# Kernel tuning notes

Hardware: AMD Instinct MI355X
Metric: run time of the kernel (lower is better)

## Reference

```python
import jax, jax.numpy as jnp
import numpy as np

N = 10000        # num_nodes
F_IN = 256       # dataset_num_features
H = 128          # hidden_channels
C_OUT = 40       # dataset_num_classes
L = 3            # num_layers
HEADS = 8
DH = H // HEADS  # per-head dim
E = 160000       # num edges (before self loops)
SCALE = 1.0 / float(np.sqrt(DH))


def setup_inputs() -> dict:
    key = jax.random.key(0)
    ks = jax.random.split(key, 8)
    s = lambda k, *sh: (jax.random.normal(k, sh, dtype=jnp.float32) * 0.05)
    return dict(
        edge_index=jax.random.randint(ks[0], (2, E), 0, N, dtype=jnp.int32),
        x_param=s(ks[1], N, F_IN),
        lin1_w=s(ks[2], F_IN, H),
        lin1_b=jnp.zeros((H,), jnp.float32),
        wq=s(ks[3], L, H, H),
        wk=s(ks[4], L, H, H),
        wv=s(ks[5], L, H, H),
        bq=jnp.zeros((L, H), jnp.float32),
        bk=jnp.zeros((L, H), jnp.float32),
        bv=jnp.zeros((L, H), jnp.float32),
        lin2_w=s(ks[6], H, C_OUT),
        lin2_b=jnp.zeros((C_OUT,), jnp.float32),
    )


def _gcn_norm(edge_index):
    # PyG gcn_norm: add self loops (weight 1), symmetric D^-1/2 A D^-1/2
    loops = jnp.arange(N, dtype=edge_index.dtype)
    row = jnp.concatenate([edge_index[0], loops])  # source j
    col = jnp.concatenate([edge_index[1], loops])  # target i
    deg = jax.ops.segment_sum(jnp.ones(row.shape, jnp.float32), col, num_segments=N)
    dis = jnp.where(deg > 0, jax.lax.rsqrt(jnp.maximum(deg, 1e-12)), 0.0)
    return row, col, dis[row] * dis[col]


def _restricted_softmax(score):
    # softmax with an implicit extra logit at `margin=0`
    m = jnp.maximum(jnp.max(score, axis=-1, keepdims=True), 0.0)
    e = jnp.exp(score - m)
    return e / (jnp.sum(e, axis=-1, keepdims=True) + jnp.exp(-m))


def _forward(edge_index, x_param, lin1_w, lin1_b, wq, wk, wv, bq, bk, bv, lin2_w, lin2_b):
    row, col, norm = _gcn_norm(edge_index)
    # dropouts are eval-mode no-ops
    x = jax.nn.relu(x_param @ lin1_w + lin1_b)  # [N, H]
    x_all = x[:, None, :]                       # [N, 1, H]
    for l in range(L):
        t = x_all.shape[1]
        # project per-node first (linear commutes with per-edge gather)
        q = (x_all[:, -1] @ wq[l] + bq[l]).reshape(N, HEADS, DH)      # query from latest state
        k = (x_all @ wk[l] + bk[l]).reshape(N, t, HEADS, DH)          # keys over full history
        v = (x_all @ wv[l] + bv[l]).reshape(N, t, HEADS, DH)
        qe = q[col]   # [Etot, heads, dh]   (x_i)
        ke = k[row]   # [Etot, t, heads, dh] (x_j)
        ve = v[row]
        score = jnp.einsum('ehd,ethd->eht', qe, ke) * SCALE
        attn = _restricted_softmax(score)        # attention-dropout is a no-op in eval
        msg = jnp.einsum('eht,ethd->ehd', attn, ve).reshape(-1, H) * norm[:, None]
        out = jax.ops.segment_sum(msg, col, num_segments=N)  # aggr='add'
        x = jax.nn.relu(out)
        x_all = jnp.concatenate([x_all, x[:, None, :]], axis=1)
    logits = x_all[:, -1] @ lin2_w + lin2_b
    return jax.nn.log_softmax(logits, axis=1)


def reference(edge_index, x_param, lin1_w, lin1_b, wq, wk, wv, bq, bk, bv, lin2_w, lin2_b):
    return _forward(edge_index, x_param, lin1_w, lin1_b, wq, wk, wv, bq, bk, bv, lin2_w, lin2_b)
```

## Files before the change

### kernel.cpp

```cpp
#include <hip/hip_runtime.h>
#include <math.h>

#define N_NODES 10000
#define F_IN_D  256
#define H_DIM   128
#define C_OUTD  40
#define NHEADS  8
#define NEDGES  160000
#define ETOT    (NEDGES + N_NODES)
#define SCALE_F 0.25f
#define TILES_N 157

typedef __attribute__((ext_vector_type(8))) short bf16x8;
typedef __attribute__((ext_vector_type(4))) float f32x4;
typedef __attribute__((ext_vector_type(2))) float f32x2;

__device__ __forceinline__ unsigned short f2bf(float f) {
    unsigned int u = __float_as_uint(f);
    unsigned int r = (u + 0x7FFFu + ((u >> 16) & 1u)) >> 16;
    return (unsigned short)r;
}
__device__ __forceinline__ float bf2f(unsigned short h) {
    return __uint_as_float(((unsigned int)h) << 16);
}
__device__ __forceinline__ unsigned char f2fp8(float v) {
    int pk = __builtin_amdgcn_cvt_pk_fp8_f32(v, v, 0, false);
    return (unsigned char)(pk & 0xff);
}


__global__ void k_scan(int* __restrict__ degi, int* __restrict__ offsets) {
    __shared__ int part[1024];
    int tid = threadIdx.x;
    int s = 0;
    if (tid < 1000) {
        int beg = tid * 10;
        #pragma unroll
        for (int i = 0; i < 10; ++i) s += degi[beg + i] + 1;
    }
    part[tid] = s;
    __syncthreads();
    for (int off = 1; off < 1024; off <<= 1) {
        int v = 0;
        if (tid >= off) v = part[tid - off];
        __syncthreads();
        part[tid] += v;
        __syncthreads();
    }
    if (tid < 1000) {
        int base = part[tid] - s;
        int beg = tid * 10;
        #pragma unroll
        for (int i = 0; i < 10; ++i) {
            int d = degi[beg + i] + 1;
            offsets[beg + i] = base;
            degi[beg + i]    = d;
            base += d;
        }
    }
}

__global__ void k_scatter(const int* __restrict__ row, const int* __restrict__ col,
                          const int* __restrict__ degi, const int* __restrict__ offsets,
                          int* cursor, int* csr_row, float* csr_norm) {
    int e = blockIdx.x * 256 + threadIdx.x;
    if (e >= ETOT) return;
    int r, c;
    if (e < NEDGES) { r = row[e]; c = col[e]; }
    else            { r = c = e - NEDGES; }
    int slot = offsets[c] + atomicAdd(&cursor[c], 1);
    float dr = rsqrtf((float)degi[r]);
    float dc = rsqrtf((float)degi[c]);
    csr_row[slot]  = r;
    csr_norm[slot] = dr * dc;
}


__global__ void k_prep(const float* __restrict__ w1, const float* __restrict__ wq,
                       const float* __restrict__ wk, const float* __restrict__ wv,
                       const float* __restrict__ w2, const int* __restrict__ col,
                       unsigned short* __restrict__ W1T, unsigned short* __restrict__ WTq,
                       unsigned short* __restrict__ WTk, unsigned short* __restrict__ WTv,
                       unsigned short* __restrict__ W2T, int* __restrict__ degi) {
    int b = blockIdx.x;
    if (b < 728) {
        int e = b * 256 + threadIdx.x;
        if (e < 32768) {
            int n = e >> 8, k = e & 255;
            W1T[e] = f2bf(w1[k * H_DIM + n]);
        } else if (e < 180224) {
            int e2 = e - 32768;
            int mat = e2 >> 14;
            int r   = e2 & 16383;
            int n = r >> 7, k = r & 127;
            int l = mat / 3, ws = mat % 3;
            const float*    src = (ws == 0) ? wq  : (ws == 1) ? wk  : wv;
            unsigned short* dst = (ws == 0) ? WTq : (ws == 1) ? WTk : WTv;
            dst[l * 16384 + n * H_DIM + k] = f2bf(src[l * 16384 + k * H_DIM + n]);
        } else if (e < 186368) {
            int e3 = e - 180224;
            int c = e3 >> 7, k = e3 & 127;
            W2T[c * H_DIM + k] = (c < C_OUTD) ? f2bf(w2[k * C_OUTD + c]) : 0;
        }
    } else {
        int e = (b - 728) * 256 + threadIdx.x;
        if (e < NEDGES) atomicAdd(&degi[col[e]], 1);
    }
}


__global__ __launch_bounds__(256) void k_lin1_mfma(const float* __restrict__ X,
                                                   const unsigned short* __restrict__ W1T,
                                                   const float* __restrict__ b1,
                                                   unsigned short* __restrict__ X0,
                                                   int nct) {
    int tid = threadIdx.x;
    int wid = tid >> 6, lane = tid & 63;
    int m = lane & 15, quad = lane >> 4;
    int rowA = blockIdx.x * 64 + wid * 16 + m;
    int rowc = rowA < N_NODES ? rowA : N_NODES - 1;
    bf16x8 af[8];
    const float* ap = X + (size_t)rowc * F_IN_D + quad * 8;
    #pragma unroll
    for (int s = 0; s < 8; ++s) {
        float4 lo = *(const float4*)(ap + s * 32);
        float4 hi = *(const float4*)(ap + s * 32 + 4);
        union { unsigned short u[8]; bf16x8 v; } pk;
        pk.u[0] = f2bf(lo.x); pk.u[1] = f2bf(lo.y);
        pk.u[2] = f2bf(lo.z); pk.u[3] = f2bf(lo.w);
        pk.u[4] = f2bf(hi.x); pk.u[5] = f2bf(hi.y);
        pk.u[6] = f2bf(hi.z); pk.u[7] = f2bf(hi.w);
        af[s] = pk.v;
    }
    int row0 = blockIdx.x * 64 + wid * 16 + quad * 4;
    for (int ct = 0; ct < nct; ++ct) {
        int col = ct * 16 + m;
        const unsigned short* bp = W1T + (size_t)col * F_IN_D + quad * 8;
        f32x4 acc = {0.f, 0.f, 0.f, 0.f};
        #pragma unroll
        for (int s = 0; s < 8; ++s) {
            bf16x8 bfr = __builtin_bit_cast(bf16x8, *(const uint4*)(bp + s * 32));
            acc = __builtin_amdgcn_mfma_f32_16x16x32_bf16(af[s], bfr, acc, 0, 0, 0);
        }
        float bb = b1[col];
        #pragma unroll
        for (int rg = 0; rg < 4; ++rg) {
            int r = row0 + rg;
            if (r < N_NODES)
                X0[(size_t)r * H_DIM + col] = f2bf(fmaxf(acc[rg] + bb, 0.f));
        }
    }
}


__global__ __launch_bounds__(256) void k_qkv_mfma(const unsigned short* __restrict__ XHb,
                                                  const unsigned short* __restrict__ WTq,
                                                  const unsigned short* __restrict__ WTk,
                                                  const unsigned short* __restrict__ WTv,
                                                  const float* __restrict__ bq,
                                                  const float* __restrict__ bk,
                                                  const float* __restrict__ bv,
                                                  unsigned short* __restrict__ Qb,
                                                  unsigned char* __restrict__ KVb,
                                                  int l, int t, int nct) {
    int tid = threadIdx.x;
    int wid = tid >> 6, lane = tid & 63;
    int m = lane & 15, quad = lane >> 4;
    int mi = blockIdx.x / TILES_N;
    int rt = blockIdx.x % TILES_N;
    const unsigned short* WT; const float* bias; int slice, mode;
    if (mi == 0)      { WT = WTq; bias = bq; slice = l;          mode = 0; }
    else if (mi <= t) { WT = WTk; bias = bk; slice = mi - 1;     mode = 1; }
    else              { WT = WTv; bias = bv; slice = mi - t - 1; mode = 2; }
    const unsigned short* A = XHb + (size_t)slice * N_NODES * H_DIM;
    int rowA = rt * 64 + wid * 16 + m;
    bf16x8 af[4];
    const unsigned short* ap = A + (size_t)rowA * H_DIM + quad * 8;
    #pragma unroll
    for (int s = 0; s < 4; ++s)
        af[s] = __builtin_bit_cast(bf16x8, *(const uint4*)(ap + s * 32));
    int row0 = rt * 64 + wid * 16 + quad * 4;
    int vofs = (mode == 2) ? 8 : 0;
    for (int cp = 0; cp < nct; ++cp) {
        int colA = cp * 32 + m;
        int colB = colA + 16;
        const unsigned short* bpA = WT + (size_t)colA * H_DIM + quad * 8;
        const unsigned short* bpB = WT + (size_t)colB * H_DIM + quad * 8;
        bf16x8 bA[4], bB[4];
        #pragma unroll
        for (int s = 0; s < 4; ++s) {
            bA[s] = __builtin_bit_cast(bf16x8, *(const uint4*)(bpA + s * 32));
            bB[s] = __builtin_bit_cast(bf16x8, *(const uint4*)(bpB + s * 32));
        }
        f32x4 accA = {0.f, 0.f, 0.f, 0.f};
        f32x4 accB = {0.f, 0.f, 0.f, 0.f};
        #pragma unroll
        for (int s = 0; s < 4; ++s) {
            accA = __builtin_amdgcn_mfma_f32_16x16x32_bf16(af[s], bA[s], accA, 0, 0, 0);
            accB = __builtin_amdgcn_mfma_f32_16x16x32_bf16(af[s], bB[s], accB, 0, 0, 0);
        }
        float bbA = bias[colA], bbB = bias[colB];
        #pragma unroll
        for (int rg = 0; rg < 4; ++rg) {
            int r = row0 + rg;
            if (r < N_NODES) {
                float vA = accA[rg] + bbA;
                float vB = accB[rg] + bbB;
                if (mode == 0) {
                    Qb[(size_t)r * H_DIM + colA] = f2bf(vA);
                    Qb[(size_t)r * H_DIM + colB] = f2bf(vB);
                } else {
                    size_t nb = ((size_t)r * 3 + slice) * 256;
                    KVb[nb + (colA >> 3) * 16 + (colA & 7) + vofs] = f2fp8(vA);
                    KVb[nb + (colB >> 3) * 16 + (colB & 7) + vofs] = f2fp8(vB);
                }
            }
        }
    }
}


template <int T>
__device__ __forceinline__ void kv_load(const uint4* __restrict__ KV, int r, int ci,
                                        uint4 (&kv)[T]) {
    const uint4* p = KV + (size_t)r * 48 + ci;
    #pragma unroll
    for (int s = 0; s < T; ++s) kv[s] = p[s * 16];
}

template <int T>
__device__ __forceinline__ void edge_accum(const uint4 (&kv)[T], const float (&q)[8],
                                           float nrm, float (&a)[8]) {
    float sc[T];
    #pragma unroll
    for (int s = 0; s < T; ++s) {
        f32x2 k0 = __builtin_amdgcn_cvt_pk_f32_fp8(kv[s].x, false);
        f32x2 k1 = __builtin_amdgcn_cvt_pk_f32_fp8(kv[s].x, true);
        f32x2 k2 = __builtin_amdgcn_cvt_pk_f32_fp8(kv[s].y, false);
        f32x2 k3 = __builtin_amdgcn_cvt_pk_f32_fp8(kv[s].y, true);
        float p = q[0] * k0[0] + q[1] * k0[1] + q[2] * k1[0] + q[3] * k1[1]
                + q[4] * k2[0] + q[5] * k2[1] + q[6] * k3[0] + q[7] * k3[1];
        p += __shfl_xor(p, 1, 2);
        sc[s] = p;
    }
    float m = 0.f;
    #pragma unroll
    for (int s = 0; s < T; ++s) m = fmaxf(m, sc[s]);
    float den = __expf(-m);
    float mv[8];
    #pragma unroll
    for (int i = 0; i < 8; ++i) mv[i] = 0.f;
    #pragma unroll
    for (int s = 0; s < T; ++s) {
        float w = __expf(sc[s] - m);
        den += w;
        f32x2 v0 = __builtin_amdgcn_cvt_pk_f32_fp8(kv[s].z, false);
        f32x2 v1 = __builtin_amdgcn_cvt_pk_f32_fp8(kv[s].z, true);
        f32x2 v2 = __builtin_amdgcn_cvt_pk_f32_fp8(kv[s].w, false);
        f32x2 v3 = __builtin_amdgcn_cvt_pk_f32_fp8(kv[s].w, true);
        mv[0] += w * v0[0]; mv[1] += w * v0[1];
        mv[2] += w * v1[0]; mv[3] += w * v1[1];
        mv[4] += w * v2[0]; mv[5] += w * v2[1];
        mv[6] += w * v3[0]; mv[7] += w * v3[1];
    }
    float ws = __fdividef(nrm, den);
    #pragma unroll
    for (int i = 0; i < 8; ++i) a[i] += ws * mv[i];
}

template <int T>
__global__ __launch_bounds__(256) void k_attn_agg(const unsigned short* __restrict__ Q,
                                                  const uint4* __restrict__ KV,
                                                  const int* __restrict__ csr_row,
                                                  const float* __restrict__ csr_norm,
                                                  const int* __restrict__ offsets,
                                                  const int* __restrict__ degi,
                                                  unsigned int* __restrict__ Xout) {
    int tid = threadIdx.x;
    int wid = tid >> 6, lane = tid & 63;
    int quarter = lane >> 4, ci = lane & 15;
    int n = blockIdx.x * 4 + wid;
    float q[8];
    {
        uint4 qp = *(const uint4*)&Q[(size_t)n * H_DIM + ci * 8];
        q[0] = __uint_as_float(qp.x << 16) * SCALE_F;
        q[1] = __uint_as_float(qp.x & 0xffff0000u) * SCALE_F;
        q[2] = __uint_as_float(qp.y << 16) * SCALE_F;
        q[3] = __uint_as_float(qp.y & 0xffff0000u) * SCALE_F;
        q[4] = __uint_as_float(qp.z << 16) * SCALE_F;
        q[5] = __uint_as_float(qp.z & 0xffff0000u) * SCALE_F;
        q[6] = __uint_as_float(qp.w << 16) * SCALE_F;
        q[7] = __uint_as_float(qp.w & 0xffff0000u) * SCALE_F;
    }
    int start = offsets[n];
    int cnt   = degi[n];
    int nq = (cnt + 3) >> 2;
    float a[8];
    #pragma unroll
    for (int i = 0; i < 8; ++i) a[i] = 0.f;

    auto rowload = [&](int j, int& r, float& nrm) {
        int j4 = j * 4 + quarter;
        int valid = j4 < cnt;
        int idx = start + (valid ? j4 : 0);
        r = csr_row[idx];
        nrm = valid ? csr_norm[idx] : 0.f;
    };

    int r0; float nCUR; rowload(0, r0, nCUR);
    int rN; float nN;   rowload(1, rN, nN);
    uint4 kvA[T], kvB[T];
    kv_load<T>(KV, r0, ci, kvA);

    int j = 0;
    for (;;) {
        {
            int r2; float n2; rowload(j + 2, r2, n2);
            kv_load<T>(KV, rN, ci, kvB);
            edge_accum<T>(kvA, q, nCUR, a);
            nCUR = nN; rN = r2; nN = n2;
        }
        if (++j >= nq) break;
        {
            int r2; float n2; rowload(j + 2, r2, n2);
            kv_load<T>(KV, rN, ci, kvA);
            edge_accum<T>(kvB, q, nCUR, a);
            nCUR = nN; rN = r2; nN = n2;
        }
        if (++j >= nq) break;
    }

    #pragma unroll
    for (int i = 0; i < 8; ++i) {
        a[i] += __shfl_xor(a[i], 16, 64);
        a[i] += __shfl_xor(a[i], 32, 64);
    }
    if (quarter == 0) {
        uint4 o;
        o.x = ((unsigned int)f2bf(fmaxf(a[1], 0.f)) << 16) | (unsigned int)f2bf(fmaxf(a[0], 0.f));
        o.y = ((unsigned int)f2bf(fmaxf(a[3], 0.f)) << 16) | (unsigned int)f2bf(fmaxf(a[2], 0.f));
        o.z = ((unsigned int)f2bf(fmaxf(a[5], 0.f)) << 16) | (unsigned int)f2bf(fmaxf(a[4], 0.f));
        o.w = ((unsigned int)f2bf(fmaxf(a[7], 0.f)) << 16) | (unsigned int)f2bf(fmaxf(a[6], 0.f));
        *(uint4*)&Xout[(size_t)n * 64 + ci * 4] = o;
    }
}


__global__ __launch_bounds__(256) void k_lin2_mfma(const unsigned short* __restrict__ X,
                                                   const unsigned short* __restrict__ W2T,
                                                   const float* __restrict__ b2,
                                                   float* __restrict__ out) {
    int tid = threadIdx.x;
    int wid = tid >> 6, lane = tid & 63;
    int m = lane & 15, quad = lane >> 4;
    int rowA = blockIdx.x * 64 + wid * 16 + m;
    bf16x8 af[4];
    const unsigned short* ap = X + (size_t)rowA * H_DIM + quad * 8;
    #pragma unroll
    for (int s = 0; s < 4; ++s)
        af[s] = __builtin_bit_cast(bf16x8, *(const uint4*)(ap + s * 32));

    f32x4 acc0 = {0.f, 0.f, 0.f, 0.f};
    f32x4 acc1 = {0.f, 0.f, 0.f, 0.f};
    f32x4 acc2 = {0.f, 0.f, 0.f, 0.f};
    const unsigned short* bp0 = W2T + (size_t)(m)      * H_DIM + quad * 8;
    const unsigned short* bp1 = W2T + (size_t)(16 + m) * H_DIM + quad * 8;
    const unsigned short* bp2 = W2T + (size_t)(32 + m) * H_DIM + quad * 8;
    #pragma unroll
    for (int s = 0; s < 4; ++s) {
        bf16x8 b0 = __builtin_bit_cast(bf16x8, *(const uint4*)(bp0 + s * 32));
        acc0 = __builtin_amdgcn_mfma_f32_16x16x32_bf16(af[s], b0, acc0, 0, 0, 0);
        bf16x8 b1 = __builtin_bit_cast(bf16x8, *(const uint4*)(bp1 + s * 32));
        acc1 = __builtin_amdgcn_mfma_f32_16x16x32_bf16(af[s], b1, acc1, 0, 0, 0);
        bf16x8 b2f = __builtin_bit_cast(bf16x8, *(const uint4*)(bp2 + s * 32));
        acc2 = __builtin_amdgcn_mfma_f32_16x16x32_bf16(af[s], b2f, acc2, 0, 0, 0);
    }

    float bb0 = b2[m], bb1 = b2[16 + m];
    float bb2 = (m < 8) ? b2[32 + m] : 0.f;
    int row0 = blockIdx.x * 64 + wid * 16 + quad * 4;
    #pragma unroll
    for (int rg = 0; rg < 4; ++rg) {
        int r = row0 + rg;
        float v0 = acc0[rg] + bb0;
        float v1 = acc1[rg] + bb1;
        float v2 = (m < 8) ? (acc2[rg] + bb2) : -INFINITY;
        float mx = fmaxf(fmaxf(v0, v1), v2);
        #pragma unroll
        for (int o = 8; o > 0; o >>= 1) mx = fmaxf(mx, __shfl_xor(mx, o, 16));
        float sm = __expf(v0 - mx) + __expf(v1 - mx) + ((m < 8) ? __expf(v2 - mx) : 0.f);
        #pragma unroll
        for (int o = 8; o > 0; o >>= 1) sm += __shfl_xor(sm, o, 16);
        float lse = mx + __logf(sm);
        if (r < N_NODES) {
            out[(size_t)r * C_OUTD + m]      = v0 - lse;
            out[(size_t)r * C_OUTD + 16 + m] = v1 - lse;
            if (m < 8) out[(size_t)r * C_OUTD + 32 + m] = v2 - lse;
        }
    }
}


extern "C" void kernel_launch(void* const* d_in, const int* in_sizes, int n_in,
                              void* d_out, int out_size, void* d_ws, size_t ws_size,
                              hipStream_t stream) {
    const int*   ei      = (const int*)d_in[0];
    const int*   row     = ei;
    const int*   col     = ei + NEDGES;
    const float* x_param = (const float*)d_in[1];
    const float* lin1_w  = (const float*)d_in[2];
    const float* lin1_b  = (const float*)d_in[3];
    const float* wq      = (const float*)d_in[4];
    const float* wk      = (const float*)d_in[5];
    const float* wv      = (const float*)d_in[6];
    const float* bq      = (const float*)d_in[7];
    const float* bk      = (const float*)d_in[8];
    const float* bv      = (const float*)d_in[9];
    const float* lin2_w  = (const float*)d_in[10];
    const float* lin2_b  = (const float*)d_in[11];
    float*       out     = (float*)d_out;

    char* wbase = (char*)d_ws;
    size_t off = 0;
    auto alloc = [&](size_t bytes) -> void* {
        off = (off + 255) & ~(size_t)255;
        void* p = wbase + off;
        off += bytes;
        return p;
    };
    int*            degi     = (int*)           alloc((size_t)N_NODES * 4);
    int*            cursor   = (int*)           alloc((size_t)N_NODES * 4);
    int*            offsets  = (int*)           alloc((size_t)N_NODES * 4);
    int*            csr_row  = (int*)           alloc((size_t)ETOT * 4);
    float*          csr_norm = (float*)         alloc((size_t)ETOT * 4);
    unsigned short* W1T      = (unsigned short*)alloc((size_t)H_DIM * F_IN_D * 2);
    unsigned short* WTq      = (unsigned short*)alloc((size_t)3 * H_DIM * H_DIM * 2);
    unsigned short* WTk      = (unsigned short*)alloc((size_t)3 * H_DIM * H_DIM * 2);
    unsigned short* WTv      = (unsigned short*)alloc((size_t)3 * H_DIM * H_DIM * 2);
    unsigned short* W2T      = (unsigned short*)alloc((size_t)48 * H_DIM * 2);
    unsigned short* XHb      = (unsigned short*)alloc((size_t)4 * N_NODES * H_DIM * 2);
    unsigned short* Qb       = (unsigned short*)alloc((size_t)N_NODES * H_DIM * 2);
    unsigned char*  KVb      = (unsigned char*) alloc((size_t)N_NODES * 3 * 256);

    hipMemsetAsync(degi, 0,
                   (size_t)((char*)(cursor + N_NODES) - (char*)degi), stream);
    k_prep<<<1353, 256, 0, stream>>>(lin1_w, wq, wk, wv, lin2_w, col,
                                     W1T, WTq, WTk, WTv, W2T, degi);
    k_scan   <<<1, 1024, 0, stream>>>(degi, offsets);
    k_scatter<<<(ETOT + 255) / 256, 256, 0, stream>>>(row, col, degi, offsets, cursor,
                                                      csr_row, csr_norm);

    k_lin1_mfma<<<TILES_N, 256, 0, stream>>>(x_param, W1T, lin1_b, XHb, 8);

    for (int l = 0; l < 3; ++l) {
        int t = l + 1;
        k_qkv_mfma<<<(1 + 2 * t) * TILES_N, 256, 0, stream>>>(
            XHb, WTq + (size_t)l * 16384, WTk + (size_t)l * 16384, WTv + (size_t)l * 16384,
            bq + l * H_DIM, bk + l * H_DIM, bv + l * H_DIM,
            Qb, KVb, l, t, 4);
        unsigned int* Xnext = (unsigned int*)(XHb + (size_t)(l + 1) * N_NODES * H_DIM);
        if (t == 1)
            k_attn_agg<1><<<2500, 256, 0, stream>>>(Qb, (const uint4*)KVb, csr_row,
                                                    csr_norm, offsets, degi, Xnext);
        else if (t == 2)
            k_attn_agg<2><<<2500, 256, 0, stream>>>(Qb, (const uint4*)KVb, csr_row,
                                                    csr_norm, offsets, degi, Xnext);
        else
            k_attn_agg<3><<<2500, 256, 0, stream>>>(Qb, (const uint4*)KVb, csr_row,
                                                    csr_norm, offsets, degi, Xnext);
    }

    k_lin2_mfma<<<TILES_N, 256, 0, stream>>>(XHb + (size_t)3 * N_NODES * H_DIM,
                                             W2T, lin2_b, out);
}
```

Before: 247.2 us.

## Fuse independent stages into shared launches and precompute history K/V during attention

Independent work is now co-scheduled inside single grids. The degree scan runs alongside lin1, the CSR scatter runs alongside the layer-0 QKV projection, and the K/V projections of older history slices for the next layer run alongside the current attention aggregation. A double-buffered KV region makes that last overlap possible, so each following QKV launch only projects the newest slice. The aim is fewer serial launches, less idle GPU time, and less redundant projection work. The cost is more complex block-index dispatch, twice the KV buffer memory, and a scan shrunk to one 256-thread block that processes 40 nodes per thread serially.

```diff
diff --git a/kernel.cpp b/kernel.cpp
--- a/kernel.cpp
+++ b/kernel.cpp
@@ -10,6 +10,7 @@
 #define ETOT    (NEDGES + N_NODES)
 #define SCALE_F 0.25f
 #define TILES_N 157
+#define KVSZ    ((size_t)N_NODES * 3 * 256)
 
 typedef __attribute__((ext_vector_type(8))) short bf16x8;
 typedef __attribute__((ext_vector_type(4))) float f32x4;
@@ -26,53 +27,6 @@
 __device__ __forceinline__ unsigned char f2fp8(float v) {
     int pk = __builtin_amdgcn_cvt_pk_fp8_f32(v, v, 0, false);
     return (unsigned char)(pk & 0xff);
-}
-
-
-__global__ void k_scan(int* __restrict__ degi, int* __restrict__ offsets) {
-    __shared__ int part[1024];
-    int tid = threadIdx.x;
-    int s = 0;
-    if (tid < 1000) {
-        int beg = tid * 10;
-        #pragma unroll
-        for (int i = 0; i < 10; ++i) s += degi[beg + i] + 1;
-    }
-    part[tid] = s;
-    __syncthreads();
-    for (int off = 1; off < 1024; off <<= 1) {
-        int v = 0;
-        if (tid >= off) v = part[tid - off];
-        __syncthreads();
-        part[tid] += v;
-        __syncthreads();
-    }
-    if (tid < 1000) {
-        int base = part[tid] - s;
-        int beg = tid * 10;
-        #pragma unroll
-        for (int i = 0; i < 10; ++i) {
-            int d = degi[beg + i] + 1;
-            offsets[beg + i] = base;
-            degi[beg + i]    = d;
-            base += d;
-        }
-    }
-}
-
-__global__ void k_scatter(const int* __restrict__ row, const int* __restrict__ col,
-                          const int* __restrict__ degi, const int* __restrict__ offsets,
-                          int* cursor, int* csr_row, float* csr_norm) {
-    int e = blockIdx.x * 256 + threadIdx.x;
-    if (e >= ETOT) return;
-    int r, c;
-    if (e < NEDGES) { r = row[e]; c = col[e]; }
-    else            { r = c = e - NEDGES; }
-    int slot = offsets[c] + atomicAdd(&cursor[c], 1);
-    float dr = rsqrtf((float)degi[r]);
-    float dc = rsqrtf((float)degi[c]);
-    csr_row[slot]  = r;
-    csr_norm[slot] = dr * dc;
 }
 
 
@@ -109,15 +63,14 @@
 }
 
 
-__global__ __launch_bounds__(256) void k_lin1_mfma(const float* __restrict__ X,
-                                                   const unsigned short* __restrict__ W1T,
-                                                   const float* __restrict__ b1,
-                                                   unsigned short* __restrict__ X0,
-                                                   int nct) {
+__device__ __forceinline__ void lin1_block(int bid, const float* __restrict__ X,
+                                           const unsigned short* __restrict__ W1T,
+                                           const float* __restrict__ b1,
+                                           unsigned short* __restrict__ X0, int nct) {
     int tid = threadIdx.x;
     int wid = tid >> 6, lane = tid & 63;
     int m = lane & 15, quad = lane >> 4;
-    int rowA = blockIdx.x * 64 + wid * 16 + m;
+    int rowA = bid * 64 + wid * 16 + m;
     int rowc = rowA < N_NODES ? rowA : N_NODES - 1;
     bf16x8 af[8];
     const float* ap = X + (size_t)rowc * F_IN_D + quad * 8;
@@ -132,7 +85,7 @@
         pk.u[6] = f2bf(hi.z); pk.u[7] = f2bf(hi.w);
         af[s] = pk.v;
     }
-    int row0 = blockIdx.x * 64 + wid * 16 + quad * 4;
+    int row0 = bid * 64 + wid * 16 + quad * 4;
     for (int ct = 0; ct < nct; ++ct) {
         int col = ct * 16 + m;
         const unsigned short* bp = W1T + (size_t)col * F_IN_D + quad * 8;
@@ -152,26 +105,27 @@
     }
 }
 
-
-__global__ __launch_bounds__(256) void k_qkv_mfma(const unsigned short* __restrict__ XHb,
-                                                  const unsigned short* __restrict__ WTq,
-                                                  const unsigned short* __restrict__ WTk,
-                                                  const unsigned short* __restrict__ WTv,
-                                                  const float* __restrict__ bq,
-                                                  const float* __restrict__ bk,
-                                                  const float* __restrict__ bv,
-                                                  unsigned short* __restrict__ Qb,
-                                                  unsigned char* __restrict__ KVb,
-                                                  int l, int t, int nct) {
+__device__ __forceinline__ void qkv_block(int mi, int rt,
+                                          const unsigned short* __restrict__ XHb,
+                                          const unsigned short* __restrict__ WTq_l,
+                                          const unsigned short* __restrict__ WTk_l,
+                                          const unsigned short* __restrict__ WTv_l,
+                                          const float* __restrict__ bq_l,
+                                          const float* __restrict__ bk_l,
+                                          const float* __restrict__ bv_l,
+                                          unsigned short* __restrict__ Qb,
+                                          unsigned char* __restrict__ KVb,
+                                          int hasQ, int qslice, int nK, int sbase, int nct) {
     int tid = threadIdx.x;
     int wid = tid >> 6, lane = tid & 63;
     int m = lane & 15, quad = lane >> 4;
-    int mi = blockIdx.x / TILES_N;
-    int rt = blockIdx.x % TILES_N;
     const unsigned short* WT; const float* bias; int slice, mode;
-    if (mi == 0)      { WT = WTq; bias = bq; slice = l;          mode = 0; }
-    else if (mi <= t) { WT = WTk; bias = bk; slice = mi - 1;     mode = 1; }
-    else              { WT = WTv; bias = bv; slice = mi - t - 1; mode = 2; }
+    if (hasQ && mi == 0) { WT = WTq_l; bias = bq_l; slice = qslice; mode = 0; }
+    else {
+        int j = mi - hasQ;
+        if (j < nK) { WT = WTk_l; bias = bk_l; slice = sbase + j;      mode = 1; }
+        else        { WT = WTv_l; bias = bv_l; slice = sbase + j - nK; mode = 2; }
+    }
     const unsigned short* A = XHb + (size_t)slice * N_NODES * H_DIM;
     int rowA = rt * 64 + wid * 16 + m;
     bf16x8 af[4];
@@ -269,17 +223,17 @@
 }
 
 template <int T>
-__global__ __launch_bounds__(256) void k_attn_agg(const unsigned short* __restrict__ Q,
-                                                  const uint4* __restrict__ KV,
-                                                  const int* __restrict__ csr_row,
-                                                  const float* __restrict__ csr_norm,
-                                                  const int* __restrict__ offsets,
-                                                  const int* __restrict__ degi,
-                                                  unsigned int* __restrict__ Xout) {
+__device__ __forceinline__ void attn_block(int bid, const unsigned short* __restrict__ Q,
+                                           const uint4* __restrict__ KV,
+                                           const int* __restrict__ csr_row,
+                                           const float* __restrict__ csr_norm,
+                                           const int* __restrict__ offsets,
+                                           const int* __restrict__ degi,
+                                           unsigned int* __restrict__ Xout) {
     int tid = threadIdx.x;
     int wid = tid >> 6, lane = tid & 63;
     int quarter = lane >> 4, ci = lane & 15;
-    int n = blockIdx.x * 4 + wid;
+    int n = bid * 4 + wid;
     float q[8];
     {
         uint4 qp = *(const uint4*)&Q[(size_t)n * H_DIM + ci * 8];
@@ -343,6 +297,132 @@
         o.w = ((unsigned int)f2bf(fmaxf(a[7], 0.f)) << 16) | (unsigned int)f2bf(fmaxf(a[6], 0.f));
         *(uint4*)&Xout[(size_t)n * 64 + ci * 4] = o;
     }
+}
+
+
+__global__ __launch_bounds__(256) void k_scan_lin1(int* __restrict__ degi,
+                                                   int* __restrict__ offsets,
+                                                   const float* __restrict__ X,
+                                                   const unsigned short* __restrict__ W1T,
+                                                   const float* __restrict__ b1,
+                                                   unsigned short* __restrict__ X0, int nct) {
+    if (blockIdx.x == 0) {
+        __shared__ int part[256];
+        int tid = threadIdx.x;
+        int s = 0;
+        if (tid < 250) {
+            const int4* d4 = (const int4*)degi;
+            for (int i = 0; i < 10; ++i) {
+                int4 v = d4[tid * 10 + i];
+                s += v.x + v.y + v.z + v.w + 4;
+            }
+        }
+        part[tid] = s;
+        __syncthreads();
+        for (int off = 1; off < 256; off <<= 1) {
+            int v = 0;
+            if (tid >= off) v = part[tid - off];
+            __syncthreads();
+            part[tid] += v;
+            __syncthreads();
+        }
+        if (tid < 250) {
+            int base = part[tid] - s;
+            int beg = tid * 40;
+            for (int i = 0; i < 40; ++i) {
+                int d = degi[beg + i] + 1;
+                offsets[beg + i] = base;
+                degi[beg + i]    = d;
+                base += d;
+            }
+        }
+        return;
+    }
+    lin1_block(blockIdx.x - 1, X, W1T, b1, X0, nct);
+}
+
+__global__ __launch_bounds__(256) void k_scatter_qkv0(const int* __restrict__ row,
+                                                      const int* __restrict__ col,
+                                                      const int* __restrict__ degi,
+                                                      const int* __restrict__ offsets,
+                                                      int* __restrict__ cursor,
+                                                      int* __restrict__ csr_row,
+                                                      float* __restrict__ csr_norm,
+                                                      const unsigned short* __restrict__ XHb,
+                                                      const unsigned short* __restrict__ WTq,
+                                                      const unsigned short* __restrict__ WTk,
+                                                      const unsigned short* __restrict__ WTv,
+                                                      const float* __restrict__ bq,
+                                                      const float* __restrict__ bk,
+                                                      const float* __restrict__ bv,
+                                                      unsigned short* __restrict__ Qb,
+                                                      unsigned char* __restrict__ KVb,
+                                                      int nct) {
+    if (blockIdx.x < 665) {
+        int e = blockIdx.x * 256 + threadIdx.x;
+        if (e >= ETOT) return;
+        int r, c;
+        if (e < NEDGES) { r = row[e]; c = col[e]; }
+        else            { r = c = e - NEDGES; }
+        int slot = offsets[c] + atomicAdd(&cursor[c], 1);
+        float dr = rsqrtf((float)degi[r]);
+        float dc = rsqrtf((float)degi[c]);
+        csr_row[slot]  = r;
+        csr_norm[slot] = dr * dc;
+        return;
+    }
+    int b = blockIdx.x - 665;
+    qkv_block(b / TILES_N, b % TILES_N, XHb, WTq, WTk, WTv, bq, bk, bv,
+              Qb, KVb, 1, 0, 1, 0, nct);
+}
+
+template <int T>
+__global__ __launch_bounds__(256) void k_attn_qkvold(const unsigned short* __restrict__ Q,
+                                                     const uint4* __restrict__ KV,
+                                                     const int* __restrict__ csr_row,
+                                                     const float* __restrict__ csr_norm,
+                                                     const int* __restrict__ offsets,
+                                                     const int* __restrict__ degi,
+                                                     unsigned int* __restrict__ Xout,
+                                                     const unsigned short* __restrict__ XHb,
+                                                     const unsigned short* __restrict__ WTk_l,
+                                                     const unsigned short* __restrict__ WTv_l,
+                                                     const float* __restrict__ bk_l,
+                                                     const float* __restrict__ bv_l,
+                                                     unsigned char* __restrict__ KVnext,
+                                                     int nK, int nct) {
+    if (blockIdx.x < 2500) {
+        attn_block<T>(blockIdx.x, Q, KV, csr_row, csr_norm, offsets, degi, Xout);
+        return;
+    }
+    int b = blockIdx.x - 2500;
+    qkv_block(b / TILES_N, b % TILES_N, XHb, nullptr, WTk_l, WTv_l,
+              nullptr, bk_l, bv_l, nullptr, KVnext, 0, 0, nK, 0, nct);
+}
+
+__global__ __launch_bounds__(256) void k_qkv(const unsigned short* __restrict__ XHb,
+                                             const unsigned short* __restrict__ WTq_l,
+                                             const unsigned short* __restrict__ WTk_l,
+                                             const unsigned short* __restrict__ WTv_l,
+                                             const float* __restrict__ bq_l,
+                                             const float* __restrict__ bk_l,
+                                             const float* __restrict__ bv_l,
+                                             unsigned short* __restrict__ Qb,
+                                             unsigned char* __restrict__ KVb,
+                                             int qslice, int nct) {
+    qkv_block(blockIdx.x / TILES_N, blockIdx.x % TILES_N, XHb, WTq_l, WTk_l, WTv_l,
+              bq_l, bk_l, bv_l, Qb, KVb, 1, qslice, 1, qslice, nct);
+}
+
+template <int T>
+__global__ __launch_bounds__(256) void k_attn_agg(const unsigned short* __restrict__ Q,
+                                                  const uint4* __restrict__ KV,
+                                                  const int* __restrict__ csr_row,
+                                                  const float* __restrict__ csr_norm,
+                                                  const int* __restrict__ offsets,
+                                                  const int* __restrict__ degi,
+                                                  unsigned int* __restrict__ Xout) {
+    attn_block<T>(blockIdx.x, Q, KV, csr_row, csr_norm, offsets, degi, Xout);
 }
 
 
@@ -440,35 +520,43 @@
     unsigned short* W2T      = (unsigned short*)alloc((size_t)48 * H_DIM * 2);
     unsigned short* XHb      = (unsigned short*)alloc((size_t)4 * N_NODES * H_DIM * 2);
     unsigned short* Qb       = (unsigned short*)alloc((size_t)N_NODES * H_DIM * 2);
-    unsigned char*  KVb      = (unsigned char*) alloc((size_t)N_NODES * 3 * 256);
+    unsigned char*  KVb      = (unsigned char*) alloc(2 * KVSZ);
 
     hipMemsetAsync(degi, 0,
                    (size_t)((char*)(cursor + N_NODES) - (char*)degi), stream);
     k_prep<<<1353, 256, 0, stream>>>(lin1_w, wq, wk, wv, lin2_w, col,
                                      W1T, WTq, WTk, WTv, W2T, degi);
-    k_scan   <<<1, 1024, 0, stream>>>(degi, offsets);
-    k_scatter<<<(ETOT + 255) / 256, 256, 0, stream>>>(row, col, degi, offsets, cursor,
-                                                      csr_row, csr_norm);
-
-    k_lin1_mfma<<<TILES_N, 256, 0, stream>>>(x_param, W1T, lin1_b, XHb, 8);
-
-    for (int l = 0; l < 3; ++l) {
-        int t = l + 1;
-        k_qkv_mfma<<<(1 + 2 * t) * TILES_N, 256, 0, stream>>>(
-            XHb, WTq + (size_t)l * 16384, WTk + (size_t)l * 16384, WTv + (size_t)l * 16384,
-            bq + l * H_DIM, bk + l * H_DIM, bv + l * H_DIM,
-            Qb, KVb, l, t, 4);
-        unsigned int* Xnext = (unsigned int*)(XHb + (size_t)(l + 1) * N_NODES * H_DIM);
-        if (t == 1)
-            k_attn_agg<1><<<2500, 256, 0, stream>>>(Qb, (const uint4*)KVb, csr_row,
-                                                    csr_norm, offsets, degi, Xnext);
-        else if (t == 2)
-            k_attn_agg<2><<<2500, 256, 0, stream>>>(Qb, (const uint4*)KVb, csr_row,
-                                                    csr_norm, offsets, degi, Xnext);
-        else
-            k_attn_agg<3><<<2500, 256, 0, stream>>>(Qb, (const uint4*)KVb, csr_row,
-                                                    csr_norm, offsets, degi, Xnext);
-    }
+
+    k_scan_lin1<<<158, 256, 0, stream>>>(degi, offsets, x_param, W1T, lin1_b, XHb, 8);
+
+    k_scatter_qkv0<<<665 + 3 * TILES_N, 256, 0, stream>>>(
+        row, col, degi, offsets, cursor, csr_row, csr_norm,
+        XHb, WTq, WTk, WTv, bq, bk, bv, Qb, KVb, 4);
+
+    unsigned int* X1 = (unsigned int*)(XHb + (size_t)1 * N_NODES * H_DIM);
+    unsigned int* X2 = (unsigned int*)(XHb + (size_t)2 * N_NODES * H_DIM);
+    unsigned int* X3 = (unsigned int*)(XHb + (size_t)3 * N_NODES * H_DIM);
+
+    k_attn_qkvold<1><<<2500 + 2 * TILES_N, 256, 0, stream>>>(
+        Qb, (const uint4*)KVb, csr_row, csr_norm, offsets, degi, X1,
+        XHb, WTk + 16384, WTv + 16384, bk + H_DIM, bv + H_DIM,
+        KVb + KVSZ, 1, 4);
+
+    k_qkv<<<3 * TILES_N, 256, 0, stream>>>(
+        XHb, WTq + 16384, WTk + 16384, WTv + 16384,
+        bq + H_DIM, bk + H_DIM, bv + H_DIM, Qb, KVb + KVSZ, 1, 4);
+
+    k_attn_qkvold<2><<<2500 + 4 * TILES_N, 256, 0, stream>>>(
+        Qb, (const uint4*)(KVb + KVSZ), csr_row, csr_norm, offsets, degi, X2,
+        XHb, WTk + 2 * 16384, WTv + 2 * 16384, bk + 2 * H_DIM, bv + 2 * H_DIM,
+        KVb, 2, 4);
+
+    k_qkv<<<3 * TILES_N, 256, 0, stream>>>(
+        XHb, WTq + 2 * 16384, WTk + 2 * 16384, WTv + 2 * 16384,
+        bq + 2 * H_DIM, bk + 2 * H_DIM, bv + 2 * H_DIM, Qb, KVb, 2, 4);
+
+    k_attn_agg<3><<<2500, 256, 0, stream>>>(Qb, (const uint4*)KVb, csr_row,
+                                            csr_norm, offsets, degi, X3);
 
     k_lin2_mfma<<<TILES_N, 256, 0, stream>>>(XHb + (size_t)3 * N_NODES * H_DIM,
                                              W2T, lin2_b, out);
```

After: 236.5 us. -4.3%, faster.
